# Kernel tuning notes

Measured on AMD Instinct MI355X. Metric: run time of the kernel, lower is better.

## Reference

```python
import jax, jax.numpy as jnp
import numpy as np

LAYERS = 3
N_NODES = 100000
N_EDGES = 800000
EMB = 100
EPS = 1e-12  # F.normalize default eps


def setup_inputs() -> dict:
    key = jax.random.key(0)
    ks = jax.random.split(key, 7)
    embedding = jax.random.normal(ks[0], (N_NODES, EMB), dtype=jnp.float32)
    adj_val = jax.random.uniform(ks[1], (N_EDGES,), dtype=jnp.float32)
    w_att = jax.random.normal(ks[2], (EMB, 1), dtype=jnp.float32) * 0.1
    b_att = jax.random.normal(ks[3], (1,), dtype=jnp.float32) * 0.1
    w_items = jax.random.normal(ks[4], (LAYERS, EMB, EMB), dtype=jnp.float32) * 0.1
    adj_row = jax.random.randint(ks[5], (N_EDGES,), 0, N_NODES, dtype=jnp.int32)
    adj_col = jax.random.randint(ks[6], (N_EDGES,), 0, N_NODES, dtype=jnp.int32)
    return {"embedding": embedding, "adj_val": adj_val, "w_att": w_att,
            "b_att": b_att, "w_items": w_items, "adj_row": adj_row, "adj_col": adj_col}


def reference(embedding, adj_val, w_att, b_att, w_items, adj_row, adj_col):
    n = embedding.shape[0]
    # column-degree normalization: adjacency.multiply(1/adjacency.sum(axis=0))
    degree = jax.ops.segment_sum(adj_val, adj_col, num_segments=n)  # [N]
    vals = adj_val / degree[adj_col]  # per-edge normalized value

    x = embedding
    final = embedding
    for i in range(LAYERS):
        scores = x @ w_att + b_att              # [N,1]
        attw = jax.nn.softmax(scores, axis=0)   # softmax over nodes (dim=0)
        x = x @ w_items[i].T                    # nn.Linear (no bias)
        m = x * attw                            # attention-weighted features
        # sparse mm: out[r] = sum_{edges e: row[e]=r} vals[e] * m[col[e]]
        gathered = m[adj_col] * vals[:, None]   # [E, EMB]
        x = jax.ops.segment_sum(gathered, adj_row, num_segments=n)
        # F.normalize(p=2, dim=-1)
        norm = jnp.linalg.norm(x, axis=-1, keepdims=True)
        x = x / jnp.maximum(norm, EPS)
        final = final + x
    return final / (LAYERS + 1)
```

## Files before the change

kernel.cpp:

```cpp
#include <hip/hip_runtime.h>
#include <hip/hip_bf16.h>

#define NN 100000
#define NE 800000
#define EM 100
#define NL 3

typedef short bf16x8 __attribute__((ext_vector_type(8)));
typedef float f32x4  __attribute__((ext_vector_type(4)));
typedef unsigned long long u64;

static constexpr size_t OFF_XB   = 0;
static constexpr size_t OFF_M    = OFF_XB   + (size_t)NN*128*2;
static constexpr size_t OFF_F    = OFF_M    + (size_t)NN*128*2;
static constexpr size_t OFF_DEG  = OFF_F    + (size_t)NN*EM*2;
static constexpr size_t OFF_SC   = OFF_DEG  + (size_t)NN*4;
static constexpr size_t OFF_ES   = OFF_SC   + (size_t)NN*4;
static constexpr size_t OFF_CNT  = OFF_ES   + (size_t)NE*8;
static constexpr size_t OFF_RP   = OFF_CNT  + (size_t)NN*4;
static constexpr size_t OFF_CUR  = OFF_RP   + (size_t)(NN+64)*4;
static constexpr size_t OFF_DGF  = OFF_CUR  + (size_t)NN*4;
static constexpr size_t OFF_BS   = OFF_DGF  + (size_t)NN*8;
static constexpr size_t OFF_BIN  = OFF_BS   + 512;
static constexpr size_t OFF_FLAG = OFF_BIN  + 32768;
static constexpr size_t OFF_WAT  = OFF_FLAG + 16;
static constexpr size_t OFF_WBF  = OFF_WAT  + 512;

#define DEG_SCALE  4294967296.0f
#define DEG_INV    (1.0f/4294967296.0f)
#define BIN_SCALE  1048576.0f
#define BIN_INV    (1.0f/1048576.0f)

__device__ inline float ldf(const void* p, int i, int f32) {
    return f32 ? ((const float*)p)[i]
               : __bfloat162float(((const __hip_bfloat16*)p)[i]);
}

__device__ inline float bflo(unsigned int u) { return __uint_as_float(u << 16); }
__device__ inline float bfhi(unsigned int u) { return __uint_as_float(u & 0xFFFF0000u); }
__device__ inline unsigned int pack2bf(float a, float b) {
    __hip_bfloat16 ha = __float2bfloat16(a), hb = __float2bfloat16(b);
    unsigned short ua = *(unsigned short*)&ha, ub = *(unsigned short*)&hb;
    return (unsigned int)ua | ((unsigned int)ub << 16);
}

__device__ inline int probe_block(const void* p, int nsamp) {
    __shared__ int sflag;
    int tid = threadIdx.x;
    if (tid < 64) {
        const unsigned short* h = (const unsigned short*)p;
        int big = 0;
        for (int i = tid; i < nsamp; i += 64) {
            int ex = (h[2 * i] >> 7) & 0xFF;
            big += (ex >= 134) ? 1 : 0;
        }
        #pragma unroll
        for (int off = 32; off; off >>= 1) big += __shfl_xor(big, off);
        if (tid == 0) sflag = (big >= 2) ? 1 : 0;
    }
    __syncthreads();
    int f = sflag;
    __syncthreads();
    return f;
}

__global__ __launch_bounds__(256) void k_setup(const void* w_att, const void* w_itm,
                                               u64* degfix, int* counts, u64* bins,
                                               float* wat, unsigned short* wbf) {
    int fw = probe_block(w_att, 50);
    int fi = probe_block(w_itm, 256);
    int i = blockIdx.x * 256 + threadIdx.x;
    if (i < NN) { degfix[i] = 0ull; counts[i] = 0; }
    if (i < 4096) bins[i] = 0ull;
    if (i < 128) wat[i] = (i < EM) ? ldf(w_att, i, fw) : 0.f;
    if (i < NL * 112 * 128) {
        int l = i / (112 * 128), rem = i % (112 * 128);
        int n = rem >> 7, k = rem & 127;
        float v = (n < EM && k < EM) ? ldf(w_itm, (l * EM + n) * EM + k, fi) : 0.f;
        __hip_bfloat16 b = __float2bfloat16(v);
        wbf[i] = *(unsigned short*)&b;
    }
}

__global__ __launch_bounds__(256) void k_initxf(const void* __restrict__ emb,
                                                const float* __restrict__ wat,
                                                unsigned int* __restrict__ xbf,
                                                unsigned int* __restrict__ fin,
                                                float* __restrict__ scores, int* flags,
                                                u64* __restrict__ bins) {
    __shared__ float sb[4];
    int femb = probe_block(emb, 256);
    if (blockIdx.x == 0 && threadIdx.x == 0) flags[0] = femb;
    int lane = threadIdx.x & 63, w = threadIdx.x >> 6;
    int r = blockIdx.x * 4 + w;
    float f0 = 0.f, f1 = 0.f, part = 0.f;
    bool act = lane < 50;
    if (act) {
        if (femb) {
            float2 t = ((const float2*)emb)[(size_t)r * 50 + lane];
            f0 = t.x; f1 = t.y;
        } else {
            unsigned int u = ((const unsigned int*)emb)[(size_t)r * 50 + lane];
            f0 = bflo(u); f1 = bfhi(u);
        }
        float2 wv = *(const float2*)(wat + 2 * lane);
        part = f0 * wv.x + f1 * wv.y;
        fin[(size_t)r * 50 + lane] = pack2bf(f0, f1);
    }
    xbf[(size_t)r * 64 + lane] = act ? pack2bf(f0, f1) : 0u;
    #pragma unroll
    for (int off = 32; off; off >>= 1) part += __shfl_xor(part, off);
    if (lane == 0) {
        float p = expf(part);
        scores[r] = p;
        sb[w] = p;
    }
    __syncthreads();
    if (threadIdx.x == 0) {
        float t = sb[0] + sb[1] + sb[2] + sb[3];
        atomicAdd(&bins[blockIdx.x & 1023], (u64)llrintf(t * BIN_SCALE));
    }
}

__global__ __launch_bounds__(256) void k_deg(const void* __restrict__ val,
                                             const int* __restrict__ row, const int* __restrict__ col,
                                             u64* degfix, int* counts) {
    int fav = probe_block(val, 256);
    int e = blockIdx.x * 256 + threadIdx.x;
    if (e >= NE) return;
    float v = ldf(val, e, fav);
    atomicAdd(&degfix[col[e]], (u64)llrintf(v * DEG_SCALE));
    atomicAdd(&counts[row[e]], 1);
}

__global__ __launch_bounds__(256) void k_scanA(const int* __restrict__ counts, int* excl, int* bsum,
                                               const u64* __restrict__ degfix, float* __restrict__ deg) {
    __shared__ int s[256];
    int base = blockIdx.x * 1024;
    int tid = threadIdx.x;
    int v[4]; int t = 0;
    #pragma unroll
    for (int i = 0; i < 4; i++) {
        int idx = base + tid * 4 + i;
        v[i] = (idx < NN) ? counts[idx] : 0;
        if (idx < NN) deg[idx] = (float)degfix[idx] * DEG_INV;
        t += v[i];
    }
    s[tid] = t; __syncthreads();
    for (int off = 1; off < 256; off <<= 1) {
        int add = (tid >= off) ? s[tid - off] : 0;
        __syncthreads();
        s[tid] += add;
        __syncthreads();
    }
    int ex = (tid == 0) ? 0 : s[tid - 1];
    #pragma unroll
    for (int i = 0; i < 4; i++) {
        int idx = base + tid * 4 + i;
        if (idx < NN) excl[idx] = ex;
        ex += v[i];
    }
    if (tid == 255) bsum[blockIdx.x] = s[255];
}

__global__ __launch_bounds__(256) void k_scanC(int* rowptr, int* cursor, const int* __restrict__ bsum) {
    __shared__ int spfx;
    int tid = threadIdx.x;
    int gi = blockIdx.x >> 2;
    if (tid < 64) {
        int t = (tid < gi) ? bsum[tid] : 0;
        if (tid + 64 < gi) t += bsum[tid + 64];
        #pragma unroll
        for (int off = 32; off; off >>= 1) t += __shfl_xor(t, off);
        if (tid == 0) spfx = t;
    }
    __syncthreads();
    int pfx = spfx;
    int i = blockIdx.x * 256 + tid;
    if (i < NN) {
        int v = rowptr[i] + pfx;
        rowptr[i] = v; cursor[i] = v;
        if (i == 0) rowptr[NN] = NE;
    }
}

__global__ __launch_bounds__(256) void k_scatter(const int* __restrict__ row, const int* __restrict__ col,
                                                 const void* __restrict__ aval,
                                                 int* cursor, int2* es) {
    int fav = probe_block(aval, 256);
    int e = blockIdx.x * 256 + threadIdx.x;
    if (e >= NE) return;
    int r = row[e];
    int c = col[e];
    int pos = atomicAdd(&cursor[r], 1);
    es[pos] = make_int2(c, __float_as_int(ldf(aval, e, fav)));
}

__global__ __launch_bounds__(256) void k_gemm(const unsigned short* __restrict__ xbf,
                                              const unsigned short* __restrict__ wbf,
                                              const float* __restrict__ scores,
                                              const u64* __restrict__ bins,
                                              const float* __restrict__ deg,
                                              unsigned short* __restrict__ m, int layer) {
    int wid = threadIdx.x >> 6, lane = threadIdx.x & 63;
    int row0 = blockIdx.x * 64 + wid * 16;
    if (row0 >= NN) return;
    int c15 = lane & 15, quad = lane >> 4;

    u64 bs = 0;
    const u64* bp = bins + (size_t)layer * 1024;
    #pragma unroll
    for (int t = 0; t < 16; t++) bs += bp[t * 64 + lane];
    #pragma unroll
    for (int off = 32; off; off >>= 1) bs += __shfl_xor(bs, off);
    float inv_sum = 1.0f / ((float)bs * BIN_INV);

    const bf16x8* xa = (const bf16x8*)(xbf + (size_t)(row0 + c15) * 128 + quad * 8);
    bf16x8 a[4];
    #pragma unroll
    for (int kq = 0; kq < 4; kq++) a[kq] = xa[kq * 4];

    float att[4];
    #pragma unroll
    for (int r = 0; r < 4; r++) {
        int grow = row0 + quad * 4 + r;
        float dv = deg[grow];
        float invd = dv > 0.f ? 1.0f / dv : 0.f;
        att[r] = scores[grow] * inv_sum * invd;
    }

    const bf16x8* wb = (const bf16x8*)(wbf + (size_t)layer * 112 * 128
                                       + (size_t)c15 * 128 + quad * 8);
    #pragma unroll
    for (int nt = 0; nt < 7; nt++) {
        f32x4 acc = {0.f, 0.f, 0.f, 0.f};
        #pragma unroll
        for (int kq = 0; kq < 4; kq++) {
            bf16x8 b = wb[nt * 256 + kq * 4];
            acc = __builtin_amdgcn_mfma_f32_16x16x32_bf16(a[kq], b, acc, 0, 0, 0);
        }
        int col = nt * 16 + c15;
        #pragma unroll
        for (int r = 0; r < 4; r++) {
            int grow = row0 + quad * 4 + r;
            unsigned short v = 0;
            if (col < EM) {
                __hip_bfloat16 bvv = __float2bfloat16(acc[r] * att[r]);
                v = *(unsigned short*)&bvv;
            }
            m[(size_t)grow * 128 + col] = v;
        }
    }
    #pragma unroll
    for (int r = 0; r < 4; r++) {
        int grow = row0 + quad * 4 + r;
        m[(size_t)grow * 128 + 112 + c15] = 0;
    }
}

__global__ __launch_bounds__(256) void k_spmm(const int* __restrict__ rowptr,
                                              const int2* __restrict__ es,
                                              const unsigned short* __restrict__ m,
                                              const float* __restrict__ wat,
                                              unsigned int* __restrict__ xbf,
                                              unsigned int* __restrict__ fin,
                                              float* __restrict__ scores,
                                              void* __restrict__ out, const int* flags,
                                              u64* __restrict__ bins,
                                              int layer, int last) {
    __shared__ float sb[4];
    int lane = threadIdx.x & 63;
    int w = threadIdx.x >> 6;
    int r = blockIdx.x * 4 + w;
    int slot = lane >> 4, k = lane & 15;
    int s = rowptr[r], e = rowptr[r + 1];
    const char* mq = (const char*)m;

    float acc[8] = {0.f, 0.f, 0.f, 0.f, 0.f, 0.f, 0.f, 0.f};
    for (int i = s; i < e; i += 8) {
        int i0 = i + slot, i1 = i + 4 + slot;
        int j0 = i0 < e - 1 ? i0 : e - 1;
        int j1 = i1 < e - 1 ? i1 : e - 1;
        int2 c0 = es[j0];
        int2 c1 = es[j1];
        float v0 = (i0 < e) ? __int_as_float(c0.y) : 0.f;
        float v1 = (i1 < e) ? __int_as_float(c1.y) : 0.f;
        uint4 u0 = *(const uint4*)(mq + (((size_t)c0.x) << 8) + (k << 4));
        uint4 u1 = *(const uint4*)(mq + (((size_t)c1.x) << 8) + (k << 4));
        const unsigned int* p0 = (const unsigned int*)&u0;
        const unsigned int* p1 = (const unsigned int*)&u1;
        #pragma unroll
        for (int t = 0; t < 4; t++) {
            acc[2 * t]     += v0 * bflo(p0[t]);
            acc[2 * t + 1] += v0 * bfhi(p0[t]);
        }
        #pragma unroll
        for (int t = 0; t < 4; t++) {
            acc[2 * t]     += v1 * bflo(p1[t]);
            acc[2 * t + 1] += v1 * bfhi(p1[t]);
        }
    }
    #pragma unroll
    for (int t = 0; t < 8; t++) {
        acc[t] += __shfl_xor(acc[t], 16);
        acc[t] += __shfl_xor(acc[t], 32);
    }
    float sq = 0.f;
    #pragma unroll
    for (int t = 0; t < 8; t++) sq += acc[t] * acc[t];
    #pragma unroll
    for (int off = 8; off; off >>= 1) sq += __shfl_xor(sq, off);
    float rn = 1.f / fmaxf(sqrtf(sq), 1e-12f);
    float n[8];
    #pragma unroll
    for (int t = 0; t < 8; t++) n[t] = acc[t] * rn;

    float part = 0.f;
    if (slot == 0) {
        if (!last) {
            uint4 q;
            q.x = pack2bf(n[0], n[1]); q.y = pack2bf(n[2], n[3]);
            q.z = pack2bf(n[4], n[5]); q.w = pack2bf(n[6], n[7]);
            *(uint4*)(xbf + (size_t)r * 64 + k * 4) = q;
        }
        if (k <= 12) {
            unsigned int fu[4] = {0u, 0u, 0u, 0u};
            size_t fb = (size_t)r * 50 + k * 4;
            uint2 fa = *(const uint2*)(fin + fb);
            fu[0] = fa.x; fu[1] = fa.y;
            if (k < 12) {
                uint2 fbv = *(const uint2*)(fin + fb + 2);
                fu[2] = fbv.x; fu[3] = fbv.y;
            }
            float fn[8];
            #pragma unroll
            for (int t = 0; t < 4; t++) {
                fn[2 * t]     = bflo(fu[t]) + n[2 * t];
                fn[2 * t + 1] = bfhi(fu[t]) + n[2 * t + 1];
            }
            if (!last) {
                uint2 pa, pb;
                pa.x = pack2bf(fn[0], fn[1]); pa.y = pack2bf(fn[2], fn[3]);
                pb.x = pack2bf(fn[4], fn[5]); pb.y = pack2bf(fn[6], fn[7]);
                *(uint2*)(fin + fb) = pa;
                if (k < 12) *(uint2*)(fin + fb + 2) = pb;
                float4 w0 = *(const float4*)(wat + k * 8);
                float4 w1 = *(const float4*)(wat + k * 8 + 4);
                part = n[0] * w0.x + n[1] * w0.y + n[2] * w0.z + n[3] * w0.w
                     + n[4] * w1.x + n[5] * w1.y + n[6] * w1.z + n[7] * w1.w;
            } else {
                if (flags[0]) {
                    float4 A, B;
                    A.x = fn[0] * 0.25f; A.y = fn[1] * 0.25f; A.z = fn[2] * 0.25f; A.w = fn[3] * 0.25f;
                    B.x = fn[4] * 0.25f; B.y = fn[5] * 0.25f; B.z = fn[6] * 0.25f; B.w = fn[7] * 0.25f;
                    float* ob = (float*)out + (size_t)r * 100 + k * 8;
                    *(float4*)ob = A;
                    if (k < 12) *(float4*)(ob + 4) = B;
                } else {
                    uint2 pa, pb;
                    pa.x = pack2bf(fn[0] * 0.25f, fn[1] * 0.25f);
                    pa.y = pack2bf(fn[2] * 0.25f, fn[3] * 0.25f);
                    pb.x = pack2bf(fn[4] * 0.25f, fn[5] * 0.25f);
                    pb.y = pack2bf(fn[6] * 0.25f, fn[7] * 0.25f);
                    unsigned int* ob = (unsigned int*)out + (size_t)r * 50 + k * 4;
                    *(uint2*)ob = pa;
                    if (k < 12) *(uint2*)(ob + 2) = pb;
                }
            }
        }
    }
    if (!last) {
        #pragma unroll
        for (int off = 8; off; off >>= 1) part += __shfl_xor(part, off);
        if (lane == 0) {
            float p = expf(part);
            scores[r] = p;
            sb[w] = p;
        }
        __syncthreads();
        if (threadIdx.x == 0) {
            float t = sb[0] + sb[1] + sb[2] + sb[3];
            atomicAdd(&bins[(size_t)(layer + 1) * 1024 + (blockIdx.x & 1023)],
                      (u64)llrintf(t * BIN_SCALE));
        }
    }
}

extern "C" void kernel_launch(void* const* d_in, const int* in_sizes, int n_in,
                              void* d_out, int out_size, void* d_ws, size_t ws_size,
                              hipStream_t stream) {
    const void* emb   = d_in[0];
    const void* aval  = d_in[1];
    const void* w_att = d_in[2];
    const void* w_itm = d_in[4];
    const int* arow = (const int*)d_in[5];
    const int* acol = (const int*)d_in[6];

    char* w = (char*)d_ws;
    unsigned int*   xbf    = (unsigned int*)(w + OFF_XB);
    unsigned short* m      = (unsigned short*)(w + OFF_M);
    unsigned int*   fin    = (unsigned int*)(w + OFF_F);
    float*          deg    = (float*)(w + OFF_DEG);
    float*          scores = (float*)(w + OFF_SC);
    int2*           es     = (int2*) (w + OFF_ES);
    int*            counts = (int*)  (w + OFF_CNT);
    int*            rowptr = (int*)  (w + OFF_RP);
    int*            cursor = (int*)  (w + OFF_CUR);
    u64*            degfix = (u64*)  (w + OFF_DGF);
    int*            bsum   = (int*)  (w + OFF_BS);
    u64*            bins   = (u64*)  (w + OFF_BIN);
    int*            flags  = (int*)  (w + OFF_FLAG);
    float*          wat    = (float*)(w + OFF_WAT);
    unsigned short* wbf    = (unsigned short*)(w + OFF_WBF);

    const int GN   = (NN + 255) / 256;
    const int GNE  = (NE + 255) / 256;
    const int GSCN = (NN + 1023) / 1024;
    const int GW4  = (NN + 3) / 4;
    const int GGE  = (NN + 63) / 64;

    k_setup<<<GN, 256, 0, stream>>>(w_att, w_itm, degfix, counts, bins, wat, wbf);
    k_initxf<<<GW4, 256, 0, stream>>>(emb, wat, xbf, fin, scores, flags, bins);
    k_deg<<<GNE, 256, 0, stream>>>(aval, arow, acol, degfix, counts);
    k_scanA<<<GSCN, 256, 0, stream>>>(counts, rowptr, bsum, degfix, deg);
    k_scanC<<<GN, 256, 0, stream>>>(rowptr, cursor, bsum);
    k_scatter<<<GNE, 256, 0, stream>>>(arow, acol, aval, cursor, es);

    for (int l = 0; l < NL; l++) {
        k_gemm<<<GGE, 256, 0, stream>>>((const unsigned short*)xbf, wbf, scores, bins, deg, m, l);
        k_spmm<<<GW4, 256, 0, stream>>>(rowptr, es, m, wat, xbf, fin, scores,
                                        d_out, flags, bins, l, (l == NL - 1) ? 1 : 0);
    }
}
```

Measured before the change: 518.0 us.

## Quantize message features to int8 per row and reuse atomic offsets in CSR scatter

```diff
diff --git a/kernel.cpp b/kernel.cpp
--- a/kernel.cpp
+++ b/kernel.cpp
@@ -12,14 +12,14 @@
 
 static constexpr size_t OFF_XB   = 0;
 static constexpr size_t OFF_M    = OFF_XB   + (size_t)NN*128*2;
-static constexpr size_t OFF_F    = OFF_M    + (size_t)NN*128*2;
+static constexpr size_t OFF_F    = OFF_M    + (size_t)NN*128;
 static constexpr size_t OFF_DEG  = OFF_F    + (size_t)NN*EM*2;
 static constexpr size_t OFF_SC   = OFF_DEG  + (size_t)NN*4;
 static constexpr size_t OFF_ES   = OFF_SC   + (size_t)NN*4;
-static constexpr size_t OFF_CNT  = OFF_ES   + (size_t)NE*8;
+static constexpr size_t OFF_POS  = OFF_ES   + (size_t)NE*8;
+static constexpr size_t OFF_CNT  = OFF_POS  + (size_t)NE*4;
 static constexpr size_t OFF_RP   = OFF_CNT  + (size_t)NN*4;
-static constexpr size_t OFF_CUR  = OFF_RP   + (size_t)(NN+64)*4;
-static constexpr size_t OFF_DGF  = OFF_CUR  + (size_t)NN*4;
+static constexpr size_t OFF_DGF  = OFF_RP   + (size_t)(NN+64)*4;
 static constexpr size_t OFF_BS   = OFF_DGF  + (size_t)NN*8;
 static constexpr size_t OFF_BIN  = OFF_BS   + 512;
 static constexpr size_t OFF_FLAG = OFF_BIN  + 32768;
@@ -43,6 +43,10 @@
     unsigned short ua = *(unsigned short*)&ha, ub = *(unsigned short*)&hb;
     return (unsigned int)ua | ((unsigned int)ub << 16);
 }
+__device__ inline float ub0(unsigned int x) { return (float)(x & 0xFF); }
+__device__ inline float ub1(unsigned int x) { return (float)((x >> 8) & 0xFF); }
+__device__ inline float ub2(unsigned int x) { return (float)((x >> 16) & 0xFF); }
+__device__ inline float ub3(unsigned int x) { return (float)(x >> 24); }
 
 __device__ inline int probe_block(const void* p, int nsamp) {
     __shared__ int sflag;
@@ -124,13 +128,13 @@
 
 __global__ __launch_bounds__(256) void k_deg(const void* __restrict__ val,
                                              const int* __restrict__ row, const int* __restrict__ col,
-                                             u64* degfix, int* counts) {
+                                             u64* degfix, int* counts, int* __restrict__ pos) {
     int fav = probe_block(val, 256);
     int e = blockIdx.x * 256 + threadIdx.x;
     if (e >= NE) return;
     float v = ldf(val, e, fav);
     atomicAdd(&degfix[col[e]], (u64)llrintf(v * DEG_SCALE));
-    atomicAdd(&counts[row[e]], 1);
+    pos[e] = atomicAdd(&counts[row[e]], 1);
 }
 
 __global__ __launch_bounds__(256) void k_scanA(const int* __restrict__ counts, int* excl, int* bsum,
@@ -163,7 +167,7 @@
     if (tid == 255) bsum[blockIdx.x] = s[255];
 }
 
-__global__ __launch_bounds__(256) void k_scanC(int* rowptr, int* cursor, const int* __restrict__ bsum) {
+__global__ __launch_bounds__(256) void k_scanC(int* rowptr, const int* __restrict__ bsum) {
     __shared__ int spfx;
     int tid = threadIdx.x;
     int gi = blockIdx.x >> 2;
@@ -178,22 +182,20 @@
     int pfx = spfx;
     int i = blockIdx.x * 256 + tid;
     if (i < NN) {
-        int v = rowptr[i] + pfx;
-        rowptr[i] = v; cursor[i] = v;
+        rowptr[i] += pfx;
         if (i == 0) rowptr[NN] = NE;
     }
 }
 
 __global__ __launch_bounds__(256) void k_scatter(const int* __restrict__ row, const int* __restrict__ col,
                                                  const void* __restrict__ aval,
-                                                 int* cursor, int2* es) {
+                                                 const int* __restrict__ rowptr,
+                                                 const int* __restrict__ pos, int2* es) {
     int fav = probe_block(aval, 256);
     int e = blockIdx.x * 256 + threadIdx.x;
     if (e >= NE) return;
-    int r = row[e];
-    int c = col[e];
-    int pos = atomicAdd(&cursor[r], 1);
-    es[pos] = make_int2(c, __float_as_int(ldf(aval, e, fav)));
+    int p = rowptr[row[e]] + pos[e];
+    es[p] = make_int2(col[e], __float_as_int(ldf(aval, e, fav)));
 }
 
 __global__ __launch_bounds__(256) void k_gemm(const unsigned short* __restrict__ xbf,
@@ -201,7 +203,7 @@
                                               const float* __restrict__ scores,
                                               const u64* __restrict__ bins,
                                               const float* __restrict__ deg,
-                                              unsigned short* __restrict__ m, int layer) {
+                                              unsigned char* __restrict__ m, int layer) {
     int wid = threadIdx.x >> 6, lane = threadIdx.x & 63;
     int row0 = blockIdx.x * 64 + wid * 16;
     if (row0 >= NN) return;
@@ -231,6 +233,7 @@
 
     const bf16x8* wb = (const bf16x8*)(wbf + (size_t)layer * 112 * 128
                                        + (size_t)c15 * 128 + quad * 8);
+    f32x4 accs[7];
     #pragma unroll
     for (int nt = 0; nt < 7; nt++) {
         f32x4 acc = {0.f, 0.f, 0.f, 0.f};
@@ -239,28 +242,34 @@
             bf16x8 b = wb[nt * 256 + kq * 4];
             acc = __builtin_amdgcn_mfma_f32_16x16x32_bf16(a[kq], b, acc, 0, 0, 0);
         }
-        int col = nt * 16 + c15;
-        #pragma unroll
-        for (int r = 0; r < 4; r++) {
-            int grow = row0 + quad * 4 + r;
-            unsigned short v = 0;
+        accs[nt] = acc;
+    }
+    #pragma unroll
+    for (int r = 0; r < 4; r++) {
+        float mx = 0.f;
+        #pragma unroll
+        for (int nt = 0; nt < 7; nt++) mx = fmaxf(mx, fabsf(accs[nt][r]));
+        #pragma unroll
+        for (int off = 1; off < 16; off <<= 1) mx = fmaxf(mx, __shfl_xor(mx, off));
+        float inv = 127.0f / fmaxf(mx, 1e-30f);
+        int grow = row0 + quad * 4 + r;
+        unsigned char* rowp = m + (size_t)grow * 128;
+        #pragma unroll
+        for (int nt = 0; nt < 7; nt++) {
+            int col = nt * 16 + c15;
             if (col < EM) {
-                __hip_bfloat16 bvv = __float2bfloat16(acc[r] * att[r]);
-                v = *(unsigned short*)&bvv;
+                int q = (int)rintf(accs[nt][r] * inv) + 128;
+                rowp[col] = (unsigned char)q;
             }
-            m[(size_t)grow * 128 + col] = v;
-        }
-    }
-    #pragma unroll
-    for (int r = 0; r < 4; r++) {
-        int grow = row0 + quad * 4 + r;
-        m[(size_t)grow * 128 + 112 + c15] = 0;
+        }
+        if (c15 == 0) *(float*)(rowp + 100) = att[r] * mx * (1.0f / 127.0f);
+        if (c15 < 6)  *(unsigned int*)(rowp + 104 + 4 * c15) = 0x80808080u;
     }
 }
 
 __global__ __launch_bounds__(256) void k_spmm(const int* __restrict__ rowptr,
                                               const int2* __restrict__ es,
-                                              const unsigned short* __restrict__ m,
+                                              const unsigned char* __restrict__ m,
                                               const float* __restrict__ wat,
                                               unsigned int* __restrict__ xbf,
                                               unsigned int* __restrict__ fin,
@@ -275,8 +284,10 @@
     int slot = lane >> 4, k = lane & 15;
     int s = rowptr[r], e = rowptr[r + 1];
     const char* mq = (const char*)m;
+    int src12 = (lane & 48) + 12;
 
     float acc[8] = {0.f, 0.f, 0.f, 0.f, 0.f, 0.f, 0.f, 0.f};
+    float tsum = 0.f;
     for (int i = s; i < e; i += 8) {
         int i0 = i + slot, i1 = i + 4 + slot;
         int j0 = i0 < e - 1 ? i0 : e - 1;
@@ -285,26 +296,34 @@
         int2 c1 = es[j1];
         float v0 = (i0 < e) ? __int_as_float(c0.y) : 0.f;
         float v1 = (i1 < e) ? __int_as_float(c1.y) : 0.f;
-        uint4 u0 = *(const uint4*)(mq + (((size_t)c0.x) << 8) + (k << 4));
-        uint4 u1 = *(const uint4*)(mq + (((size_t)c1.x) << 8) + (k << 4));
-        const unsigned int* p0 = (const unsigned int*)&u0;
-        const unsigned int* p1 = (const unsigned int*)&u1;
-        #pragma unroll
-        for (int t = 0; t < 4; t++) {
-            acc[2 * t]     += v0 * bflo(p0[t]);
-            acc[2 * t + 1] += v0 * bfhi(p0[t]);
-        }
-        #pragma unroll
-        for (int t = 0; t < 4; t++) {
-            acc[2 * t]     += v1 * bflo(p1[t]);
-            acc[2 * t + 1] += v1 * bfhi(p1[t]);
-        }
+        uint2 u0 = *(const uint2*)(mq + (((size_t)c0.x) << 7) + (k << 3));
+        uint2 u1 = *(const uint2*)(mq + (((size_t)c1.x) << 7) + (k << 3));
+        float s0 = __uint_as_float(__shfl((int)u0.y, src12));
+        float s1 = __uint_as_float(__shfl((int)u1.y, src12));
+        float t0 = v0 * s0, t1 = v1 * s1;
+        tsum += t0 + t1;
+        unsigned int x0 = u0.x, y0 = (k == 12) ? 0x80808080u : u0.y;
+        unsigned int x1 = u1.x, y1 = (k == 12) ? 0x80808080u : u1.y;
+        acc[0] += t0 * ub0(x0); acc[1] += t0 * ub1(x0);
+        acc[2] += t0 * ub2(x0); acc[3] += t0 * ub3(x0);
+        acc[4] += t0 * ub0(y0); acc[5] += t0 * ub1(y0);
+        acc[6] += t0 * ub2(y0); acc[7] += t0 * ub3(y0);
+        acc[0] += t1 * ub0(x1); acc[1] += t1 * ub1(x1);
+        acc[2] += t1 * ub2(x1); acc[3] += t1 * ub3(x1);
+        acc[4] += t1 * ub0(y1); acc[5] += t1 * ub1(y1);
+        acc[6] += t1 * ub2(y1); acc[7] += t1 * ub3(y1);
     }
     #pragma unroll
     for (int t = 0; t < 8; t++) {
         acc[t] += __shfl_xor(acc[t], 16);
         acc[t] += __shfl_xor(acc[t], 32);
     }
+    tsum += __shfl_xor(tsum, 16);
+    tsum += __shfl_xor(tsum, 32);
+    float corr = 128.0f * tsum;
+    #pragma unroll
+    for (int t = 0; t < 8; t++) acc[t] -= corr;
+
     float sq = 0.f;
     #pragma unroll
     for (int t = 0; t < 8; t++) sq += acc[t] * acc[t];
@@ -398,14 +417,14 @@
 
     char* w = (char*)d_ws;
     unsigned int*   xbf    = (unsigned int*)(w + OFF_XB);
-    unsigned short* m      = (unsigned short*)(w + OFF_M);
+    unsigned char*  m      = (unsigned char*)(w + OFF_M);
     unsigned int*   fin    = (unsigned int*)(w + OFF_F);
     float*          deg    = (float*)(w + OFF_DEG);
     float*          scores = (float*)(w + OFF_SC);
     int2*           es     = (int2*) (w + OFF_ES);
+    int*            pos    = (int*)  (w + OFF_POS);
     int*            counts = (int*)  (w + OFF_CNT);
     int*            rowptr = (int*)  (w + OFF_RP);
-    int*            cursor = (int*)  (w + OFF_CUR);
     u64*            degfix = (u64*)  (w + OFF_DGF);
     int*            bsum   = (int*)  (w + OFF_BS);
     u64*            bins   = (u64*)  (w + OFF_BIN);
@@ -421,10 +440,10 @@
 
     k_setup<<<GN, 256, 0, stream>>>(w_att, w_itm, degfix, counts, bins, wat, wbf);
     k_initxf<<<GW4, 256, 0, stream>>>(emb, wat, xbf, fin, scores, flags, bins);
-    k_deg<<<GNE, 256, 0, stream>>>(aval, arow, acol, degfix, counts);
+    k_deg<<<GNE, 256, 0, stream>>>(aval, arow, acol, degfix, counts, pos);
     k_scanA<<<GSCN, 256, 0, stream>>>(counts, rowptr, bsum, degfix, deg);
-    k_scanC<<<GN, 256, 0, stream>>>(rowptr, cursor, bsum);
-    k_scatter<<<GNE, 256, 0, stream>>>(arow, acol, aval, cursor, es);
+    k_scanC<<<GN, 256, 0, stream>>>(rowptr, bsum);
+    k_scatter<<<GNE, 256, 0, stream>>>(arow, acol, aval, rowptr, pos, es);
 
     for (int l = 0; l < NL; l++) {
         k_gemm<<<GGE, 256, 0, stream>>>((const unsigned short*)xbf, wbf, scores, bins, deg, m, l);
```

Measured after the change: 498.6 us. 3.7% less time.
